# Kernel tuning notes

Measured on AMD Instinct MI355X. Metric: run time of the kernel, lower is better.

Reference implementation:

```python
import jax, jax.numpy as jnp
import numpy as np

N, E, D, H, L = 20000, 320000, 128, 8, 3
C = D // H  # per-head channels = 16


def setup_inputs() -> dict:
    key = jax.random.key(0)
    ks = jax.random.split(key, 20)
    s = 1.0 / np.sqrt(D)
    inp = {
        "x": jax.random.normal(ks[0], (N, D), dtype=jnp.float32),
        "edge_index": jax.random.randint(ks[1], (2, E), 0, N, dtype=jnp.int64),
        "Wq": jax.random.normal(ks[2], (L, D, D), dtype=jnp.float32) * s,
        "bq": jnp.zeros((L, D), dtype=jnp.float32),
        "Wk": jax.random.normal(ks[3], (L, D, D), dtype=jnp.float32) * s,
        "bk": jnp.zeros((L, D), dtype=jnp.float32),
        "Wv": jax.random.normal(ks[4], (L, D, D), dtype=jnp.float32) * s,
        "bv": jnp.zeros((L, D), dtype=jnp.float32),
        "Wskip": jax.random.normal(ks[5], (L, D, D), dtype=jnp.float32) * s,
        "bskip": jnp.zeros((L, D), dtype=jnp.float32),
        "Wbeta": jax.random.normal(ks[6], (L, 3 * D, 1), dtype=jnp.float32) * (1.0 / np.sqrt(3 * D)),
        "ln_g": jnp.ones((L, D), dtype=jnp.float32),
        "ln_b": jnp.zeros((L, D), dtype=jnp.float32),
        "Wout": jax.random.normal(ks[7], (D, D), dtype=jnp.float32) * s,
        "bout": jnp.zeros((D,), dtype=jnp.float32),
    }
    return inp


def _layer_norm(x, g, b, eps=1e-5):
    mu = jnp.mean(x, axis=-1, keepdims=True)
    var = jnp.mean(jnp.square(x - mu), axis=-1, keepdims=True)
    return (x - mu) * jax.lax.rsqrt(var + eps) * g + b


def _transformer_conv(x, src, dst, Wq, bq, Wk, bk, Wv, bv, Wskip, bskip, Wbeta):
    # project q/k/v: [N, D] -> [N, H, C]
    q = (x @ Wq + bq).reshape(N, H, C)
    k = (x @ Wk + bk).reshape(N, H, C)
    v = (x @ Wv + bv).reshape(N, H, C)
    # per-edge attention logits: [E, H]
    alpha = jnp.sum(q[dst] * k[src], axis=-1) / np.sqrt(C)
    # scatter-softmax over edges grouped by dst node
    m = jax.ops.segment_max(alpha, dst, num_segments=N)  # [N, H]
    m = jnp.where(jnp.isfinite(m), m, 0.0)
    ea = jnp.exp(alpha - m[dst])
    denom = jax.ops.segment_sum(ea, dst, num_segments=N)  # [N, H]
    attn = ea / (denom[dst] + 1e-16)  # [E, H]
    # weighted message aggregation: [N, H, C] -> [N, D]
    out = jax.ops.segment_sum(attn[:, :, None] * v[src], dst, num_segments=N)
    out = out.reshape(N, D)
    # beta-gated skip connection (beta=True, root_weight=True)
    x_r = x @ Wskip + bskip
    beta = jax.nn.sigmoid(jnp.concatenate([out, x_r, out - x_r], axis=-1) @ Wbeta)  # [N, 1]
    return beta * x_r + (1.0 - beta) * out


def reference(x, edge_index, Wq, bq, Wk, bk, Wv, bv, Wskip, bskip, Wbeta, ln_g, ln_b, Wout, bout):
    src, dst = edge_index[0], edge_index[1]
    for i in range(L):
        residual = x
        x = _transformer_conv(x, src, dst, Wq[i], bq[i], Wk[i], bk[i], Wv[i], bv[i],
                              Wskip[i], bskip[i], Wbeta[i])
        x = jax.nn.relu(x)  # dropout is identity in eval mode
        x = _layer_norm(x + residual, ln_g[i], ln_b[i])
    return x @ Wout + bout
```

## Files before the change

kernel.cpp:

```cpp
#include <hip/hip_runtime.h>

#define N_NODES 20000
#define N_EDGES 320000
#define DIM 128
#define NLAYER 3
#define SCAN_BLK 1024
#define N_SCAN_BLKS ((N_NODES + SCAN_BLK - 1) / SCAN_BLK)
#define LDS_STRIDE 136

#define PREP_CASTW_BLKS 208
#define PREP_ZERO_BLKS 79
#define PREP_TOTAL (PREP_CASTW_BLKS + PREP_ZERO_BLKS)

typedef __attribute__((ext_vector_type(8))) short short8;
typedef __attribute__((ext_vector_type(4))) float f32x4;
typedef __attribute__((ext_vector_type(2))) float f32x2;

__device__ inline ushort f2bf(float f) {
  uint u = __float_as_uint(f);
  uint r = (u + 0x7fffu + ((u >> 16) & 1u)) >> 16;
  return (ushort)r;
}
__device__ inline float bf2f(ushort u) { return __uint_as_float(((uint)u) << 16); }

__device__ inline uint f2fp8(float f) {
  return __builtin_amdgcn_cvt_pk_fp8_f32(f, 0.f, 0, false) & 0xffu;
}
__device__ inline void fp8x4_to_f32(uint w, float* o) {
  f32x2 lo = __builtin_amdgcn_cvt_pk_f32_fp8(w, false);
  f32x2 hi = __builtin_amdgcn_cvt_pk_f32_fp8(w, true);
  o[0] = lo[0]; o[1] = lo[1]; o[2] = hi[0]; o[3] = hi[1];
}

__global__ __launch_bounds__(256) void prep_kernel(
    const float* __restrict__ Wq, const float* __restrict__ Wk,
    const float* __restrict__ Wv, const float* __restrict__ Ws,
    const float* __restrict__ Wo, ushort* __restrict__ wt,
    int* __restrict__ degc) {
  int b = blockIdx.x;
  int t = threadIdx.x;
  if (b < PREP_CASTW_BLKS) {
    int z = b >> 4;
    int r = b & 15;
    int k0 = (r >> 2) * 32, n0 = (r & 3) * 32;
    const float* src;
    if (z < 12) {
      int l = z >> 2, j = z & 3;
      src = (j == 0 ? Wq : j == 1 ? Wk : j == 2 ? Wv : Ws) + (size_t)l * DIM * DIM;
    } else {
      src = Wo;
    }
    __shared__ float tile[32][33];
    int tx = t & 31, ty = t >> 5;
    #pragma unroll
    for (int i = 0; i < 32; i += 8)
      tile[ty + i][tx] = src[(size_t)(k0 + ty + i) * DIM + n0 + tx];
    __syncthreads();
    ushort* dst = wt + (size_t)z * DIM * DIM;
    #pragma unroll
    for (int i = 0; i < 32; i += 8)
      dst[(size_t)(n0 + ty + i) * DIM + k0 + tx] = f2bf(tile[tx][ty + i]);
  } else {
    int i = (b - PREP_CASTW_BLKS) * 256 + t;
    if (i < N_NODES) degc[i] = 0;
  }
}


__global__ void count_deg_kernel(const int* __restrict__ ei, int* __restrict__ deg) {
  int e = blockIdx.x * 256 + threadIdx.x;
  if (e < N_EDGES) atomicAdd(&deg[ei[N_EDGES + e]], 1);
}

__global__ __launch_bounds__(SCAN_BLK) void scan1_kernel(const int* __restrict__ deg,
                                                         int* __restrict__ rowptr,
                                                         int* __restrict__ blksum) {
  __shared__ int wsum[16];
  int t = threadIdx.x, lane = t & 63, w = t >> 6;
  int i = blockIdx.x * SCAN_BLK + t;
  int val = (i < N_NODES) ? deg[i] : 0;
  int s = val;
  #pragma unroll
  for (int off = 1; off < 64; off <<= 1) {
    int u = __shfl_up(s, off);
    if (lane >= off) s += u;
  }
  if (lane == 63) wsum[w] = s;
  __syncthreads();
  if (t < 16) {
    int wv = wsum[t];
    int ss = wv;
    #pragma unroll
    for (int off = 1; off < 16; off <<= 1) {
      int u = __shfl_up(ss, off);
      if (t >= off) ss += u;
    }
    wsum[t] = ss - wv;
  }
  __syncthreads();
  int excl = wsum[w] + s - val;
  if (i < N_NODES) rowptr[i] = excl;
  if (t == SCAN_BLK - 1) blksum[blockIdx.x] = excl + val;
}

__global__ void scan2_kernel(int* __restrict__ blksum, int* __restrict__ rowptr) {
  int t = threadIdx.x;
  int val = (t < N_SCAN_BLKS) ? blksum[t] : 0;
  int s = val;
  #pragma unroll
  for (int off = 1; off < 64; off <<= 1) {
    int u = __shfl_up(s, off);
    if (t >= off) s += u;
  }
  if (t < N_SCAN_BLKS) blksum[t] = s - val;
  if (t == 63) rowptr[N_NODES] = s;
}

__global__ __launch_bounds__(SCAN_BLK) void scan3_kernel(int* __restrict__ rowptr,
                                                         const int* __restrict__ blksum,
                                                         int* __restrict__ degc) {
  int i = blockIdx.x * SCAN_BLK + threadIdx.x;
  if (i < N_NODES) {
    rowptr[i] += blksum[blockIdx.x];
    degc[i] = 0;
  }
}

__global__ void scatter_kernel(const int* __restrict__ ei, const int* __restrict__ rowptr,
                               int* __restrict__ cursor, int* __restrict__ csr_src) {
  int e = blockIdx.x * 256 + threadIdx.x;
  if (e < N_EDGES) {
    int d = ei[N_EDGES + e];
    int s = ei[e];
    int pos = atomicAdd(&cursor[d], 1);
    csr_src[rowptr[d] + pos] = s;
  }
}

template <int IN_F32>
__global__ __launch_bounds__(256) void gemm_mfma_kernel(
    const void* __restrict__ Xp, const ushort* __restrict__ WT,
    const float* __restrict__ B0, const float* __restrict__ B1,
    const float* __restrict__ B2, const float* __restrict__ B3,
    void* __restrict__ O0, void* __restrict__ O1, void* __restrict__ O2,
    void* __restrict__ O3, int m0, int m1, int m2, int m3) {
  __shared__ ushort As[128 * LDS_STRIDE];
  int mat = blockIdx.y;
  const ushort* Wt = WT + (size_t)mat * DIM * DIM;
  const float* bias;
  void* O;
  int mode;
  switch (mat) {
    case 0: bias = B0; O = O0; mode = m0; break;
    case 1: bias = B1; O = O1; mode = m1; break;
    case 2: bias = B2; O = O2; mode = m2; break;
    default: bias = B3; O = O3; mode = m3; break;
  }
  int t = threadIdx.x;
  int wid = t >> 6, lane = t & 63;
  int row0 = blockIdx.x * 128;
  int wr = wid >> 1, wc = wid & 1;
  int lr = lane & 15;
  int kc8 = (lane >> 4) * 8;

  if (IN_F32) {
    const float* Xf = (const float*)Xp;
    int rowi = t >> 5;
    int col4 = (t & 31) * 4;
    #pragma unroll
    for (int pass = 0; pass < 16; ++pass) {
      int row = pass * 8 + rowi;
      int gr = min(row0 + row, N_NODES - 1);
      float4 f = *(const float4*)(Xf + (size_t)gr * DIM + col4);
      ushort4 u;
      u.x = f2bf(f.x); u.y = f2bf(f.y); u.z = f2bf(f.z); u.w = f2bf(f.w);
      *(ushort4*)(As + row * LDS_STRIDE + col4) = u;
    }
  } else {
    const ushort* X = (const ushort*)Xp;
    int rowi = t >> 4;
    int col = (t & 15) * 8;
    #pragma unroll
    for (int pass = 0; pass < 8; ++pass) {
      int row = pass * 16 + rowi;
      int gr = min(row0 + row, N_NODES - 1);
      short8 val = *(const short8*)(X + (size_t)gr * DIM + col);
      *(short8*)(As + row * LDS_STRIDE + col) = val;
    }
  }
  __syncthreads();

  f32x4 acc[4][4];
  #pragma unroll
  for (int i = 0; i < 4; ++i)
    #pragma unroll
    for (int j = 0; j < 4; ++j) acc[i][j] = (f32x4){0.f, 0.f, 0.f, 0.f};

  #pragma unroll
  for (int ks = 0; ks < 4; ++ks) {
    short8 b[4];
    #pragma unroll
    for (int cf = 0; cf < 4; ++cf) {
      int c = wc * 64 + cf * 16 + lr;
      b[cf] = *(const short8*)(Wt + (size_t)c * DIM + ks * 32 + kc8);
    }
    #pragma unroll
    for (int rf = 0; rf < 4; ++rf) {
      int r = wr * 64 + rf * 16 + lr;
      short8 a = *(const short8*)(As + r * LDS_STRIDE + ks * 32 + kc8);
      #pragma unroll
      for (int cf = 0; cf < 4; ++cf)
        acc[rf][cf] = __builtin_amdgcn_mfma_f32_16x16x32_bf16(a, b[cf], acc[rf][cf], 0, 0, 0);
    }
  }

  #pragma unroll
  for (int cf = 0; cf < 4; ++cf) {
    int c = wc * 64 + cf * 16 + lr;
    float bv = bias[c];
    #pragma unroll
    for (int rf = 0; rf < 4; ++rf) {
      #pragma unroll
      for (int reg = 0; reg < 4; ++reg) {
        int r = row0 + wr * 64 + rf * 16 + (lane >> 4) * 4 + reg;
        if (r < N_NODES) {
          float val = acc[rf][cf][reg] + bv;
          if (mode == 0)
            ((ushort*)O)[(size_t)r * DIM + c] = f2bf(val);
          else if (mode == 1)
            ((float*)O)[(size_t)r * DIM + c] = val;
          else if (mode == 2)
            ((unsigned char*)O)[(size_t)r * 256 + c] = (unsigned char)f2fp8(val);
          else
            ((unsigned char*)O)[(size_t)r * 256 + 128 + c] = (unsigned char)f2fp8(val);
        }
      }
    }
  }
}

__global__ __launch_bounds__(256) void attn_fused_kernel(
    const ushort* __restrict__ q, const unsigned char* __restrict__ kv,
    const ushort* __restrict__ xr, const float* __restrict__ xres,
    const int* __restrict__ rowptr, const int* __restrict__ csr_src,
    const float* __restrict__ wbeta, const float* __restrict__ lng,
    const float* __restrict__ lnb, float* __restrict__ xnext,
    ushort* __restrict__ xnextb) {
  __shared__ float red[4][8][8][20];
  int w = threadIdx.x >> 6;
  int lane = threadIdx.x & 63;
  int n = blockIdx.x * 4 + w;
  int h = lane & 7, e = lane >> 3;

  const ushort* qrow = q + (size_t)n * DIM + h * 16;
  short8 q0 = *(const short8*)qrow;
  short8 q1 = *(const short8*)(qrow + 8);
  float qf[16];
  #pragma unroll
  for (int i = 0; i < 8; ++i) {
    qf[i] = bf2f((ushort)q0[i]) * 0.25f;
    qf[8 + i] = bf2f((ushort)q1[i]) * 0.25f;
  }

  int s0 = rowptr[n];
  int deg = rowptr[n + 1] - s0;
  float acc[16];
  #pragma unroll
  for (int i = 0; i < 16; ++i) acc[i] = 0.f;
  float dsum = 0.f;

  int src_n = (deg > 0) ? csr_src[s0 + min(e, deg - 1)] : 0;
  for (int base = 0; base < deg; base += 8) {
    int idx = base + e;
    bool valid = idx < deg;
    int src = src_n;
    if (base + 8 < deg)
      src_n = csr_src[s0 + min(base + 8 + e, deg - 1)];
    const unsigned char* rec = kv + (size_t)src * 256 + h * 16;
    uint4 ku = *(const uint4*)rec;
    uint4 vu = *(const uint4*)(rec + 128);
    float kf[16], vf[16];
    fp8x4_to_f32(ku.x, kf + 0);
    fp8x4_to_f32(ku.y, kf + 4);
    fp8x4_to_f32(ku.z, kf + 8);
    fp8x4_to_f32(ku.w, kf + 12);
    fp8x4_to_f32(vu.x, vf + 0);
    fp8x4_to_f32(vu.y, vf + 4);
    fp8x4_to_f32(vu.z, vf + 8);
    fp8x4_to_f32(vu.w, vf + 12);
    float p = 0.f;
    #pragma unroll
    for (int i = 0; i < 16; ++i) p = fmaf(qf[i], kf[i], p);
    float ea = __expf(p);
    ea = valid ? ea : 0.f;
    dsum += ea;
    #pragma unroll
    for (int i = 0; i < 16; ++i) acc[i] = fmaf(ea, vf[i], acc[i]);
  }

  {
    float* my = &red[w][e][h][0];
    *(float4*)(my + 0) = make_float4(acc[0], acc[1], acc[2], acc[3]);
    *(float4*)(my + 4) = make_float4(acc[4], acc[5], acc[6], acc[7]);
    *(float4*)(my + 8) = make_float4(acc[8], acc[9], acc[10], acc[11]);
    *(float4*)(my + 12) = make_float4(acc[12], acc[13], acc[14], acc[15]);
    my[16] = dsum;
  }
  asm volatile("s_waitcnt lgkmcnt(0)" ::: "memory");

  int c0 = lane * 2;
  int hh = lane >> 3, cc = (lane & 7) * 2;
  float o0 = 0.f, o1 = 0.f, den = 0.f;
  #pragma unroll
  for (int ee = 0; ee < 8; ++ee) {
    float2 tv = *(float2*)&red[w][ee][hh][cc];
    o0 += tv.x;
    o1 += tv.y;
    den += red[w][ee][hh][16];
  }
  float inv = 1.f / (den + 1e-16f);
  o0 *= inv;
  o1 *= inv;

  ushort2 xru = *(const ushort2*)(xr + (size_t)n * DIM + c0);
  float xr0 = bf2f(xru.x), xr1 = bf2f(xru.y);
  float wa0 = wbeta[c0] + wbeta[2 * DIM + c0];
  float wa1 = wbeta[c0 + 1] + wbeta[2 * DIM + c0 + 1];
  float wb0 = wbeta[DIM + c0] - wbeta[2 * DIM + c0];
  float wb1 = wbeta[DIM + c0 + 1] - wbeta[2 * DIM + c0 + 1];
  float bs = o0 * wa0 + o1 * wa1 + xr0 * wb0 + xr1 * wb1;
  #pragma unroll
  for (int off = 1; off < 64; off <<= 1) bs += __shfl_xor(bs, off);
  float beta = 1.f / (1.f + __expf(-bs));
  float y0 = fmaxf(beta * xr0 + (1.f - beta) * o0, 0.f);
  float y1 = fmaxf(beta * xr1 + (1.f - beta) * o1, 0.f);
  float2 rv = *(const float2*)(xres + (size_t)n * DIM + c0);
  y0 += rv.x;
  y1 += rv.y;
  float s = y0 + y1;
  #pragma unroll
  for (int off = 1; off < 64; off <<= 1) s += __shfl_xor(s, off);
  float mu = s * (1.f / 128.f);
  float d0 = y0 - mu, d1 = y1 - mu;
  float vs = d0 * d0 + d1 * d1;
  #pragma unroll
  for (int off = 1; off < 64; off <<= 1) vs += __shfl_xor(vs, off);
  float rstd = rsqrtf(vs * (1.f / 128.f) + 1e-5f);
  float2 g = *(const float2*)(lng + c0);
  float2 b = *(const float2*)(lnb + c0);
  float out0 = d0 * rstd * g.x + b.x;
  float out1 = d1 * rstd * g.y + b.y;
  *(float2*)(xnext + (size_t)n * DIM + c0) = make_float2(out0, out1);
  ushort2 ob;
  ob.x = f2bf(out0);
  ob.y = f2bf(out1);
  *(ushort2*)(xnextb + (size_t)n * DIM + c0) = ob;
}


extern "C" void kernel_launch(void* const* d_in, const int* in_sizes, int n_in,
                              void* d_out, int out_size, void* d_ws, size_t ws_size,
                              hipStream_t stream) {
  const float* x_in = (const float*)d_in[0];
  const int* ei = (const int*)d_in[1];
  const float* Wq = (const float*)d_in[2];
  const float* bq = (const float*)d_in[3];
  const float* Wk = (const float*)d_in[4];
  const float* bk = (const float*)d_in[5];
  const float* Wv = (const float*)d_in[6];
  const float* bv = (const float*)d_in[7];
  const float* Wsk = (const float*)d_in[8];
  const float* bsk = (const float*)d_in[9];
  const float* Wb = (const float*)d_in[10];
  const float* lng = (const float*)d_in[11];
  const float* lnb = (const float*)d_in[12];
  const float* Wout = (const float*)d_in[13];
  const float* bout = (const float*)d_in[14];
  float* out = (float*)d_out;

  char* p = (char*)d_ws;
  auto alloc = [&](size_t bytes) {
    char* r = p;
    p += (bytes + 255) & ~(size_t)255;
    return r;
  };
  const size_t NB2 = (size_t)N_NODES * DIM * 2;
  const size_t NB4 = (size_t)N_NODES * DIM * 4;
  ushort* xbb = (ushort*)alloc(NB2);
  ushort* qb = (ushort*)alloc(NB2);
  unsigned char* kvb = (unsigned char*)alloc((size_t)N_NODES * 256);
  ushort* xrb = (ushort*)alloc(NB2);
  float* xf0 = (float*)alloc(NB4);
  float* xf1 = (float*)alloc(NB4);
  ushort* wt = (ushort*)alloc((size_t)13 * DIM * DIM * 2);
  int* rowptr = (int*)alloc((N_NODES + 1) * 4);
  int* degc = (int*)alloc(N_NODES * 4);
  int* blksum = (int*)alloc(64 * 4);
  int* csr_src = (int*)alloc(N_EDGES * 4);

  prep_kernel<<<PREP_TOTAL, 256, 0, stream>>>(Wq, Wk, Wv, Wsk, Wout, wt, degc);

  count_deg_kernel<<<(N_EDGES + 255) / 256, 256, 0, stream>>>(ei, degc);
  scan1_kernel<<<N_SCAN_BLKS, SCAN_BLK, 0, stream>>>(degc, rowptr, blksum);
  scan2_kernel<<<1, 64, 0, stream>>>(blksum, rowptr);
  scan3_kernel<<<N_SCAN_BLKS, SCAN_BLK, 0, stream>>>(rowptr, blksum, degc);
  scatter_kernel<<<(N_EDGES + 255) / 256, 256, 0, stream>>>(ei, rowptr, degc, csr_src);

  const int GX = (N_NODES + 127) / 128;
  const float* xres = x_in;
  float* xfbufs[NLAYER] = {xf0, xf1, xf0};
  for (int l = 0; l < NLAYER; ++l) {
    if (l == 0) {
      gemm_mfma_kernel<1><<<dim3(GX, 4), 256, 0, stream>>>(
          (const void*)x_in, wt + (size_t)l * 4 * DIM * DIM,
          bq + (size_t)l * DIM, bk + (size_t)l * DIM, bv + (size_t)l * DIM,
          bsk + (size_t)l * DIM,
          qb, kvb, kvb, xrb, 0, 2, 3, 0);
    } else {
      gemm_mfma_kernel<0><<<dim3(GX, 4), 256, 0, stream>>>(
          (const void*)xbb, wt + (size_t)l * 4 * DIM * DIM,
          bq + (size_t)l * DIM, bk + (size_t)l * DIM, bv + (size_t)l * DIM,
          bsk + (size_t)l * DIM,
          qb, kvb, kvb, xrb, 0, 2, 3, 0);
    }
    attn_fused_kernel<<<N_NODES / 4, 256, 0, stream>>>(
        qb, kvb, xrb, xres, rowptr, csr_src,
        Wb + (size_t)l * 3 * DIM, lng + (size_t)l * DIM, lnb + (size_t)l * DIM,
        xfbufs[l], xbb);
    xres = xfbufs[l];
  }
  gemm_mfma_kernel<0><<<dim3(GX, 1), 256, 0, stream>>>(
      (const void*)xbb, wt + (size_t)12 * DIM * DIM, bout, bout, bout, bout,
      out, out, out, out, 1, 1, 1, 1);
}
```

Measured before the change: 198.1 us.

## Merge scan into lookback kernel, widen GEMM blocks, unroll edge loop, drop fp32 residual

Replaces the three-kernel prefix scan with a single decoupled-lookback scan that spins on per-block sums. The GEMM now runs 512-thread blocks, so each wave computes half as many row fragments. The attention edge loop processes two edges per lane per iteration to expose more memory parallelism. The fp32 residual buffer is dropped and the bf16 activation is read back as the residual, which cuts traffic but lowers precision. The attention kernel reads xbb as its residual while writing xbb in place, and the lookback spin relies on all scan blocks being co-resident.

```diff
diff --git a/kernel.cpp b/kernel.cpp
--- a/kernel.cpp
+++ b/kernel.cpp
@@ -36,7 +36,7 @@
     const float* __restrict__ Wq, const float* __restrict__ Wk,
     const float* __restrict__ Wv, const float* __restrict__ Ws,
     const float* __restrict__ Wo, ushort* __restrict__ wt,
-    int* __restrict__ degc) {
+    int* __restrict__ degc, int* __restrict__ bsum) {
   int b = blockIdx.x;
   int t = threadIdx.x;
   if (b < PREP_CASTW_BLKS) {
@@ -63,6 +63,7 @@
   } else {
     int i = (b - PREP_CASTW_BLKS) * 256 + t;
     if (i < N_NODES) degc[i] = 0;
+    else if (i < N_NODES + N_SCAN_BLKS) bsum[i - N_NODES] = 0;
   }
 }
 
@@ -72,13 +73,14 @@
   if (e < N_EDGES) atomicAdd(&deg[ei[N_EDGES + e]], 1);
 }
 
-__global__ __launch_bounds__(SCAN_BLK) void scan1_kernel(const int* __restrict__ deg,
-                                                         int* __restrict__ rowptr,
-                                                         int* __restrict__ blksum) {
+__global__ __launch_bounds__(SCAN_BLK) void scan_lookback_kernel(
+    int* __restrict__ degc, int* __restrict__ rowptr, int* __restrict__ bsum) {
   __shared__ int wsum[16];
-  int t = threadIdx.x, lane = t & 63, w = t >> 6;
-  int i = blockIdx.x * SCAN_BLK + t;
-  int val = (i < N_NODES) ? deg[i] : 0;
+  __shared__ int prevs;
+  int t = threadIdx.x, lane = t & 63, w = t >> 6, bid = blockIdx.x;
+  int i = bid * SCAN_BLK + t;
+  int val = (i < N_NODES) ? degc[i] : 0;
+  if (i < N_NODES) degc[i] = 0;
   int s = val;
   #pragma unroll
   for (int off = 1; off < 64; off <<= 1) {
@@ -99,31 +101,26 @@
   }
   __syncthreads();
   int excl = wsum[w] + s - val;
-  if (i < N_NODES) rowptr[i] = excl;
-  if (t == SCAN_BLK - 1) blksum[blockIdx.x] = excl + val;
-}
-
-__global__ void scan2_kernel(int* __restrict__ blksum, int* __restrict__ rowptr) {
-  int t = threadIdx.x;
-  int val = (t < N_SCAN_BLKS) ? blksum[t] : 0;
-  int s = val;
-  #pragma unroll
-  for (int off = 1; off < 64; off <<= 1) {
-    int u = __shfl_up(s, off);
-    if (t >= off) s += u;
-  }
-  if (t < N_SCAN_BLKS) blksum[t] = s - val;
-  if (t == 63) rowptr[N_NODES] = s;
-}
-
-__global__ __launch_bounds__(SCAN_BLK) void scan3_kernel(int* __restrict__ rowptr,
-                                                         const int* __restrict__ blksum,
-                                                         int* __restrict__ degc) {
-  int i = blockIdx.x * SCAN_BLK + threadIdx.x;
-  if (i < N_NODES) {
-    rowptr[i] += blksum[blockIdx.x];
-    degc[i] = 0;
-  }
+  if (t == SCAN_BLK - 1)
+    __hip_atomic_store(&bsum[bid], excl + val + 1, __ATOMIC_RELEASE,
+                       __HIP_MEMORY_SCOPE_AGENT);
+  if (w == 0) {
+    int p = 0;
+    for (int j = lane; j < bid; j += 64) {
+      int v;
+      do {
+        v = __hip_atomic_load(&bsum[j], __ATOMIC_ACQUIRE, __HIP_MEMORY_SCOPE_AGENT);
+      } while (v == 0);
+      p += v - 1;
+    }
+    #pragma unroll
+    for (int off = 1; off < 64; off <<= 1) p += __shfl_xor(p, off);
+    if (t == 0) prevs = p;
+  }
+  __syncthreads();
+  int off0 = prevs;
+  if (i < N_NODES) rowptr[i] = off0 + excl;
+  if (bid == N_SCAN_BLKS - 1 && t == SCAN_BLK - 1) rowptr[N_NODES] = off0 + excl + val;
 }
 
 __global__ void scatter_kernel(const int* __restrict__ ei, const int* __restrict__ rowptr,
@@ -138,7 +135,7 @@
 }
 
 template <int IN_F32>
-__global__ __launch_bounds__(256) void gemm_mfma_kernel(
+__global__ __launch_bounds__(512) void gemm_mfma_kernel(
     const void* __restrict__ Xp, const ushort* __restrict__ WT,
     const float* __restrict__ B0, const float* __restrict__ B1,
     const float* __restrict__ B2, const float* __restrict__ B3,
@@ -168,8 +165,8 @@
     int rowi = t >> 5;
     int col4 = (t & 31) * 4;
     #pragma unroll
-    for (int pass = 0; pass < 16; ++pass) {
-      int row = pass * 8 + rowi;
+    for (int pass = 0; pass < 8; ++pass) {
+      int row = pass * 16 + rowi;
       int gr = min(row0 + row, N_NODES - 1);
       float4 f = *(const float4*)(Xf + (size_t)gr * DIM + col4);
       ushort4 u;
@@ -181,8 +178,8 @@
     int rowi = t >> 4;
     int col = (t & 15) * 8;
     #pragma unroll
-    for (int pass = 0; pass < 8; ++pass) {
-      int row = pass * 16 + rowi;
+    for (int pass = 0; pass < 4; ++pass) {
+      int row = pass * 32 + rowi;
       int gr = min(row0 + row, N_NODES - 1);
       short8 val = *(const short8*)(X + (size_t)gr * DIM + col);
       *(short8*)(As + row * LDS_STRIDE + col) = val;
@@ -190,9 +187,9 @@
   }
   __syncthreads();
 
-  f32x4 acc[4][4];
-  #pragma unroll
-  for (int i = 0; i < 4; ++i)
+  f32x4 acc[2][4];
+  #pragma unroll
+  for (int i = 0; i < 2; ++i)
     #pragma unroll
     for (int j = 0; j < 4; ++j) acc[i][j] = (f32x4){0.f, 0.f, 0.f, 0.f};
 
@@ -205,8 +202,8 @@
       b[cf] = *(const short8*)(Wt + (size_t)c * DIM + ks * 32 + kc8);
     }
     #pragma unroll
-    for (int rf = 0; rf < 4; ++rf) {
-      int r = wr * 64 + rf * 16 + lr;
+    for (int rf = 0; rf < 2; ++rf) {
+      int r = wr * 32 + rf * 16 + lr;
       short8 a = *(const short8*)(As + r * LDS_STRIDE + ks * 32 + kc8);
       #pragma unroll
       for (int cf = 0; cf < 4; ++cf)
@@ -219,10 +216,10 @@
     int c = wc * 64 + cf * 16 + lr;
     float bv = bias[c];
     #pragma unroll
-    for (int rf = 0; rf < 4; ++rf) {
+    for (int rf = 0; rf < 2; ++rf) {
       #pragma unroll
       for (int reg = 0; reg < 4; ++reg) {
-        int r = row0 + wr * 64 + rf * 16 + (lane >> 4) * 4 + reg;
+        int r = row0 + wr * 32 + rf * 16 + (lane >> 4) * 4 + reg;
         if (r < N_NODES) {
           float val = acc[rf][cf][reg] + bv;
           if (mode == 0)
@@ -239,13 +236,13 @@
   }
 }
 
+template <int RES_F32>
 __global__ __launch_bounds__(256) void attn_fused_kernel(
     const ushort* __restrict__ q, const unsigned char* __restrict__ kv,
-    const ushort* __restrict__ xr, const float* __restrict__ xres,
+    const ushort* __restrict__ xr, const void* __restrict__ xres,
     const int* __restrict__ rowptr, const int* __restrict__ csr_src,
     const float* __restrict__ wbeta, const float* __restrict__ lng,
-    const float* __restrict__ lnb, float* __restrict__ xnext,
-    ushort* __restrict__ xnextb) {
+    const float* __restrict__ lnb, ushort* __restrict__ xnextb) {
   __shared__ float red[4][8][8][20];
   int w = threadIdx.x >> 6;
   int lane = threadIdx.x & 63;
@@ -264,35 +261,43 @@
 
   int s0 = rowptr[n];
   int deg = rowptr[n + 1] - s0;
+  int dm1 = deg - 1;
   float acc[16];
   #pragma unroll
   for (int i = 0; i < 16; ++i) acc[i] = 0.f;
   float dsum = 0.f;
 
-  int src_n = (deg > 0) ? csr_src[s0 + min(e, deg - 1)] : 0;
-  for (int base = 0; base < deg; base += 8) {
-    int idx = base + e;
-    bool valid = idx < deg;
-    int src = src_n;
-    if (base + 8 < deg)
-      src_n = csr_src[s0 + min(base + 8 + e, deg - 1)];
-    const unsigned char* rec = kv + (size_t)src * 256 + h * 16;
-    uint4 ku = *(const uint4*)rec;
-    uint4 vu = *(const uint4*)(rec + 128);
+  for (int base = 0; base < deg; base += 16) {
+    int i1 = base + e, i2 = base + 8 + e;
+    bool va1 = i1 < deg, va2 = i2 < deg;
+    int src1 = csr_src[s0 + min(i1, dm1)];
+    int src2 = csr_src[s0 + min(i2, dm1)];
+    const unsigned char* r1 = kv + (size_t)src1 * 256 + h * 16;
+    const unsigned char* r2 = kv + (size_t)src2 * 256 + h * 16;
+    uint4 ku1 = *(const uint4*)r1;
+    uint4 vu1 = *(const uint4*)(r1 + 128);
+    uint4 ku2 = *(const uint4*)r2;
+    uint4 vu2 = *(const uint4*)(r2 + 128);
     float kf[16], vf[16];
-    fp8x4_to_f32(ku.x, kf + 0);
-    fp8x4_to_f32(ku.y, kf + 4);
-    fp8x4_to_f32(ku.z, kf + 8);
-    fp8x4_to_f32(ku.w, kf + 12);
-    fp8x4_to_f32(vu.x, vf + 0);
-    fp8x4_to_f32(vu.y, vf + 4);
-    fp8x4_to_f32(vu.z, vf + 8);
-    fp8x4_to_f32(vu.w, vf + 12);
+    fp8x4_to_f32(ku1.x, kf + 0); fp8x4_to_f32(ku1.y, kf + 4);
+    fp8x4_to_f32(ku1.z, kf + 8); fp8x4_to_f32(ku1.w, kf + 12);
+    fp8x4_to_f32(vu1.x, vf + 0); fp8x4_to_f32(vu1.y, vf + 4);
+    fp8x4_to_f32(vu1.z, vf + 8); fp8x4_to_f32(vu1.w, vf + 12);
     float p = 0.f;
     #pragma unroll
     for (int i = 0; i < 16; ++i) p = fmaf(qf[i], kf[i], p);
-    float ea = __expf(p);
-    ea = valid ? ea : 0.f;
+    float ea = va1 ? __expf(p) : 0.f;
+    dsum += ea;
+    #pragma unroll
+    for (int i = 0; i < 16; ++i) acc[i] = fmaf(ea, vf[i], acc[i]);
+    fp8x4_to_f32(ku2.x, kf + 0); fp8x4_to_f32(ku2.y, kf + 4);
+    fp8x4_to_f32(ku2.z, kf + 8); fp8x4_to_f32(ku2.w, kf + 12);
+    fp8x4_to_f32(vu2.x, vf + 0); fp8x4_to_f32(vu2.y, vf + 4);
+    fp8x4_to_f32(vu2.z, vf + 8); fp8x4_to_f32(vu2.w, vf + 12);
+    p = 0.f;
+    #pragma unroll
+    for (int i = 0; i < 16; ++i) p = fmaf(qf[i], kf[i], p);
+    ea = va2 ? __expf(p) : 0.f;
     dsum += ea;
     #pragma unroll
     for (int i = 0; i < 16; ++i) acc[i] = fmaf(ea, vf[i], acc[i]);
@@ -334,9 +339,16 @@
   float beta = 1.f / (1.f + __expf(-bs));
   float y0 = fmaxf(beta * xr0 + (1.f - beta) * o0, 0.f);
   float y1 = fmaxf(beta * xr1 + (1.f - beta) * o1, 0.f);
-  float2 rv = *(const float2*)(xres + (size_t)n * DIM + c0);
-  y0 += rv.x;
-  y1 += rv.y;
+  float rv0, rv1;
+  if (RES_F32) {
+    float2 rv = *(const float2*)((const float*)xres + (size_t)n * DIM + c0);
+    rv0 = rv.x; rv1 = rv.y;
+  } else {
+    ushort2 ru = *(const ushort2*)((const ushort*)xres + (size_t)n * DIM + c0);
+    rv0 = bf2f(ru.x); rv1 = bf2f(ru.y);
+  }
+  y0 += rv0;
+  y1 += rv1;
   float s = y0 + y1;
   #pragma unroll
   for (int off = 1; off < 64; off <<= 1) s += __shfl_xor(s, off);
@@ -350,7 +362,6 @@
   float2 b = *(const float2*)(lnb + c0);
   float out0 = d0 * rstd * g.x + b.x;
   float out1 = d1 * rstd * g.y + b.y;
-  *(float2*)(xnext + (size_t)n * DIM + c0) = make_float2(out0, out1);
   ushort2 ob;
   ob.x = f2bf(out0);
   ob.y = f2bf(out1);
@@ -385,51 +396,46 @@
     return r;
   };
   const size_t NB2 = (size_t)N_NODES * DIM * 2;
-  const size_t NB4 = (size_t)N_NODES * DIM * 4;
   ushort* xbb = (ushort*)alloc(NB2);
   ushort* qb = (ushort*)alloc(NB2);
   unsigned char* kvb = (unsigned char*)alloc((size_t)N_NODES * 256);
   ushort* xrb = (ushort*)alloc(NB2);
-  float* xf0 = (float*)alloc(NB4);
-  float* xf1 = (float*)alloc(NB4);
   ushort* wt = (ushort*)alloc((size_t)13 * DIM * DIM * 2);
   int* rowptr = (int*)alloc((N_NODES + 1) * 4);
   int* degc = (int*)alloc(N_NODES * 4);
-  int* blksum = (int*)alloc(64 * 4);
+  int* bsum = (int*)alloc(N_SCAN_BLKS * 4);
   int* csr_src = (int*)alloc(N_EDGES * 4);
 
-  prep_kernel<<<PREP_TOTAL, 256, 0, stream>>>(Wq, Wk, Wv, Wsk, Wout, wt, degc);
-
+  prep_kernel<<<PREP_TOTAL, 256, 0, stream>>>(Wq, Wk, Wv, Wsk, Wout, wt, degc, bsum);
   count_deg_kernel<<<(N_EDGES + 255) / 256, 256, 0, stream>>>(ei, degc);
-  scan1_kernel<<<N_SCAN_BLKS, SCAN_BLK, 0, stream>>>(degc, rowptr, blksum);
-  scan2_kernel<<<1, 64, 0, stream>>>(blksum, rowptr);
-  scan3_kernel<<<N_SCAN_BLKS, SCAN_BLK, 0, stream>>>(rowptr, blksum, degc);
+  scan_lookback_kernel<<<N_SCAN_BLKS, SCAN_BLK, 0, stream>>>(degc, rowptr, bsum);
   scatter_kernel<<<(N_EDGES + 255) / 256, 256, 0, stream>>>(ei, rowptr, degc, csr_src);
 
   const int GX = (N_NODES + 127) / 128;
-  const float* xres = x_in;
-  float* xfbufs[NLAYER] = {xf0, xf1, xf0};
   for (int l = 0; l < NLAYER; ++l) {
     if (l == 0) {
-      gemm_mfma_kernel<1><<<dim3(GX, 4), 256, 0, stream>>>(
+      gemm_mfma_kernel<1><<<dim3(GX, 4), 512, 0, stream>>>(
           (const void*)x_in, wt + (size_t)l * 4 * DIM * DIM,
           bq + (size_t)l * DIM, bk + (size_t)l * DIM, bv + (size_t)l * DIM,
           bsk + (size_t)l * DIM,
           qb, kvb, kvb, xrb, 0, 2, 3, 0);
+      attn_fused_kernel<1><<<N_NODES / 4, 256, 0, stream>>>(
+          qb, kvb, xrb, (const void*)x_in, rowptr, csr_src,
+          Wb + (size_t)l * 3 * DIM, lng + (size_t)l * DIM, lnb + (size_t)l * DIM,
+          xbb);
     } else {
-      gemm_mfma_kernel<0><<<dim3(GX, 4), 256, 0, stream>>>(
+      gemm_mfma_kernel<0><<<dim3(GX, 4), 512, 0, stream>>>(
           (const void*)xbb, wt + (size_t)l * 4 * DIM * DIM,
           bq + (size_t)l * DIM, bk + (size_t)l * DIM, bv + (size_t)l * DIM,
           bsk + (size_t)l * DIM,
           qb, kvb, kvb, xrb, 0, 2, 3, 0);
-    }
-    attn_fused_kernel<<<N_NODES / 4, 256, 0, stream>>>(
-        qb, kvb, xrb, xres, rowptr, csr_src,
-        Wb + (size_t)l * 3 * DIM, lng + (size_t)l * DIM, lnb + (size_t)l * DIM,
-        xfbufs[l], xbb);
-    xres = xfbufs[l];
-  }
-  gemm_mfma_kernel<0><<<dim3(GX, 1), 256, 0, stream>>>(
+      attn_fused_kernel<0><<<N_NODES / 4, 256, 0, stream>>>(
+          qb, kvb, xrb, (const void*)xbb, rowptr, csr_src,
+          Wb + (size_t)l * 3 * DIM, lng + (size_t)l * DIM, lnb + (size_t)l * DIM,
+          xbb);
+    }
+  }
+  gemm_mfma_kernel<0><<<dim3(GX, 1), 512, 0, stream>>>(
       (const void*)xbb, wt + (size_t)12 * DIM * DIM, bout, bout, bout, bout,
       out, out, out, out, 1, 1, 1, 1);
 }
```

Measured after the change: 207.6 us. 1.05x slower.
